# Performance work log

Measured on AMD Instinct MI355X. Metric: run time of the kernel, lower is better.

The kernel has to match this reference:

```python
import jax, jax.numpy as jnp
import numpy as np

N_NODES = 100000
N_EDGES = 1600000
N_GRAPHS = 128
F_IN = 4
H = 128
OUT = 2


def setup_inputs() -> dict:
    key = jax.random.key(0)
    ks = jax.random.split(key, 32)
    inp = {}
    inp["node_attr"] = jax.random.normal(ks[0], (N_NODES, F_IN), dtype=jnp.float32)
    inp["edge_index"] = jax.random.randint(ks[1], (2, N_EDGES), 0, N_NODES, dtype=jnp.int64)
    inp["batch"] = jnp.sort(jax.random.randint(ks[2], (N_NODES,), 0, N_GRAPHS, dtype=jnp.int64))
    # GraphConv params: lin_rel (weight+bias) applied to aggregated msgs, lin_root (no bias)
    dims = [(F_IN, H), (H, H), (H, H), (H, H)]
    for i, (din, dout) in enumerate(dims):
        s = 1.0 / np.sqrt(din)
        inp[f"Wr{i}"] = jax.random.uniform(ks[3 + 3 * i], (din, dout), jnp.float32, -s, s)
        inp[f"br{i}"] = jax.random.uniform(ks[4 + 3 * i], (dout,), jnp.float32, -s, s)
        inp[f"Wo{i}"] = jax.random.uniform(ks[5 + 3 * i], (din, dout), jnp.float32, -s, s)
    s = 1.0 / np.sqrt(H)
    for j, name in enumerate(["5", "6", "7", "8"]):
        inp[f"W{name}"] = jax.random.uniform(ks[16 + 2 * j], (H, H), jnp.float32, -s, s)
        inp[f"b{name}"] = jax.random.uniform(ks[17 + 2 * j], (H,), jnp.float32, -s, s)
    inp["Wl"] = jax.random.uniform(ks[30], (H, OUT), jnp.float32, -s, s)
    inp["bl"] = jax.random.uniform(ks[31], (OUT,), jnp.float32, -s, s)
    return inp


def _graph_conv(x, src, dst, Wr, br, Wo):
    # PyG GraphConv (aggr='add'): out = lin_rel(sum_{j->i} x_j) + lin_root(x_i)
    agg = jax.ops.segment_sum(x[src], dst, num_segments=N_NODES)
    return agg @ Wr + br + x @ Wo


def reference(node_attr, edge_index, batch,
              Wr0, br0, Wo0, Wr1, br1, Wo1, Wr2, br2, Wo2, Wr3, br3, Wo3,
              W5, b5, W6, b6, W7, b7, W8, b8, Wl, bl):
    src, dst = edge_index[0], edge_index[1]
    x = node_attr
    for Wr, br, Wo in [(Wr0, br0, Wo0), (Wr1, br1, Wo1), (Wr2, br2, Wo2), (Wr3, br3, Wo3)]:
        x = jax.nn.relu(_graph_conv(x, src, dst, Wr, br, Wo))
    # global mean pool over graphs
    sums = jax.ops.segment_sum(x, batch, num_segments=N_GRAPHS)
    cnt = jax.ops.segment_sum(jnp.ones((N_NODES,), x.dtype), batch, num_segments=N_GRAPHS)
    g = sums / jnp.maximum(cnt, 1.0)[:, None]
    # dropout p=0.5 is identity in eval mode
    g = jax.nn.relu(g @ W5 + b5)
    g = jax.nn.relu(g @ W6 + b6)
    g = jax.nn.relu(g @ W7 + b7)
    g = jax.nn.relu(g @ W8 + b8)
    return jax.nn.sigmoid(g @ Wl + bl)
```

## Files before the change

kernel.cpp:

```cpp
#include <hip/hip_runtime.h>
#include <hip/hip_bf16.h>
#include <math.h>

#define NN 100000
#define NE 1600000
#define NG 128
#define H 128
#define DMAX 64
#define NB 391
#define BCAP 5120
#define EPB 3125

typedef __attribute__((ext_vector_type(8))) short short8;
typedef __attribute__((ext_vector_type(4))) float floatx4;
typedef __attribute__((ext_vector_type(2))) float floatx2;
typedef __attribute__((ext_vector_type(4))) int intx4;
typedef __attribute__((ext_vector_type(4))) unsigned uintx4;
typedef __attribute__((ext_vector_type(2))) unsigned uintx2;


__global__ void k_init_wcvt(int* __restrict__ gbase, float* __restrict__ gsum,
                            unsigned* __restrict__ rowF8a, unsigned* __restrict__ rowF8b,
                            const float* __restrict__ Wr1, const float* __restrict__ Wo1,
                            const float* __restrict__ Wr2, const float* __restrict__ Wo2,
                            const float* __restrict__ Wr3, const float* __restrict__ Wo3,
                            __hip_bfloat16* __restrict__ wf) {
  if (blockIdx.x < 384) {
    int t = blockIdx.x * 256 + threadIdx.x;
    int L = t >> 15, tt = t & 32767;
    const float* Wr = (L == 0) ? Wr1 : (L == 1) ? Wr2 : Wr3;
    const float* Wo = (L == 0) ? Wo1 : (L == 1) ? Wo2 : Wo3;
    int j = tt & 7, lanex = (tt >> 3) & 63, ct = (tt >> 9) & 7, kt = tt >> 12;
    int lr = lanex & 15, quad = lanex >> 4;
    int n = ct * 16 + lr;
    int r = kt * 32 + quad * 8 + j;
    float v = (r < 128) ? Wr[r * 128 + n] : Wo[(r - 128) * 128 + n];
    wf[t] = __float2bfloat16(v);
  } else {
    int t = (blockIdx.x - 384) * 256 + threadIdx.x;
    if (t < NB) gbase[t] = 0;
    else if (t < NB + NG * H) gsum[t - NB] = 0.f;
    else if (t < NB + NG * H + 32) rowF8a[t - NB - NG * H] = 0u;
    else if (t < NB + NG * H + 64) rowF8b[t - NB - NG * H - 32] = 0u;
  }
}

__global__ __launch_bounds__(256) void k_bucket(const int* __restrict__ ei,
                                                int* __restrict__ gbase,
                                                int2* __restrict__ pairs) {
  __shared__ int scnt[512];
  __shared__ int soff[NB];
  __shared__ int sbase[NB];
  __shared__ int2 stg[EPB];
  __shared__ short sbkt[EPB];
  const int tid = threadIdx.x;
  const int e0 = blockIdx.x * EPB;
  const int* dst = ei + NE;

  scnt[tid] = 0;
  scnt[tid + 256] = 0;
  __syncthreads();
  for (int e = e0 + tid; e < e0 + EPB; e += 256) {
    int d = __builtin_nontemporal_load(dst + e);
    atomicAdd(&scnt[d >> 8], 1);
  }
  __syncthreads();
  int c0 = scnt[tid], c1 = scnt[tid + 256];
  for (int off = 1; off < 512; off <<= 1) {
    int v0 = (tid >= off) ? scnt[tid - off] : 0;
    int v1 = (tid + 256 >= off) ? scnt[tid + 256 - off] : 0;
    __syncthreads();
    scnt[tid] += v0;
    scnt[tid + 256] += v1;
    __syncthreads();
  }
  if (tid < NB) {
    soff[tid] = scnt[tid] - c0;
    sbase[tid] = c0 ? atomicAdd(&gbase[tid], c0) : 0;
  }
  if (tid + 256 < NB) {
    soff[tid + 256] = scnt[tid + 256] - c1;
    sbase[tid + 256] = c1 ? atomicAdd(&gbase[tid + 256], c1) : 0;
  }
  __syncthreads();
  scnt[tid] = 0;
  scnt[tid + 256] = 0;
  __syncthreads();
  for (int e = e0 + tid; e < e0 + EPB; e += 256) {
    int d = __builtin_nontemporal_load(dst + e);
    int s = __builtin_nontemporal_load(ei + e);
    int b = d >> 8;
    int p = soff[b] + atomicAdd(&scnt[b], 1);
    stg[p] = make_int2(s, d);
    sbkt[p] = (short)b;
  }
  __syncthreads();
  for (int i = tid; i < EPB; i += 256) {
    int b = sbkt[i];
    int gpos = sbase[b] + (i - soff[b]);
    if (gpos < BCAP) pairs[(size_t)b * BCAP + gpos] = stg[i];
  }
}

__global__ __launch_bounds__(256) void k_fill2(const int2* __restrict__ pairs,
                                               const int* __restrict__ gbase,
                                               int* __restrict__ fcnt,
                                               int* __restrict__ colp) {
  __shared__ int scnt[256];
  const int b = blockIdx.x;
  const int d0 = b << 8;
  const int tid = threadIdx.x;
  scnt[tid] = 0;
  __syncthreads();
  int n = gbase[b];
  if (n > BCAP) n = BCAP;
  const int2* pp = pairs + (size_t)b * BCAP;
  for (int e = tid; e < n; e += 256) {
    int2 sd = pp[e];
    int dl = sd.y - d0;
    int pos = atomicAdd(&scnt[dl], 1);
    if (pos < DMAX) colp[((size_t)(d0 + dl) << 6) + pos] = sd.x;
  }
  __syncthreads();
  int d = d0 + tid;
  if (d < NN) {
    int c = scnt[tid];
    fcnt[d] = (c > DMAX) ? DMAX : c;
  }
}

__device__ inline unsigned pk_bf16(float a, float b) {
  unsigned ua = __float_as_uint(a), ub = __float_as_uint(b);
  ua = (ua + 0x7fffu + ((ua >> 16) & 1u)) >> 16;
  ub = (ub + 0x7fffu + ((ub >> 16) & 1u)) & 0xffff0000u;
  return ua | ub;
}

__device__ inline void accf8(float* a, uint2 u) {
  floatx2 p;
  p = __builtin_amdgcn_cvt_pk_f32_fp8((int)u.x, false); a[0] += p.x; a[1] += p.y;
  p = __builtin_amdgcn_cvt_pk_f32_fp8((int)u.x, true);  a[2] += p.x; a[3] += p.y;
  p = __builtin_amdgcn_cvt_pk_f32_fp8((int)u.y, false); a[4] += p.x; a[5] += p.y;
  p = __builtin_amdgcn_cvt_pk_f32_fp8((int)u.y, true);  a[6] += p.x; a[7] += p.y;
}

__device__ inline short8 f8x8_bf16(uintx2 u) {
  floatx2 p0 = __builtin_amdgcn_cvt_pk_f32_fp8((int)u.x, false);
  floatx2 p1 = __builtin_amdgcn_cvt_pk_f32_fp8((int)u.x, true);
  floatx2 p2 = __builtin_amdgcn_cvt_pk_f32_fp8((int)u.y, false);
  floatx2 p3 = __builtin_amdgcn_cvt_pk_f32_fp8((int)u.y, true);
  union { uintx4 u; short8 s; } cv;
  cv.u.x = (__float_as_uint(p0.y) & 0xffff0000u) | (__float_as_uint(p0.x) >> 16);
  cv.u.y = (__float_as_uint(p1.y) & 0xffff0000u) | (__float_as_uint(p1.x) >> 16);
  cv.u.z = (__float_as_uint(p2.y) & 0xffff0000u) | (__float_as_uint(p2.x) >> 16);
  cv.u.w = (__float_as_uint(p3.y) & 0xffff0000u) | (__float_as_uint(p3.x) >> 16);
  return cv.s;
}

__global__ void k_aggf8(const uint2* __restrict__ xf8, const int* __restrict__ fcnt,
                        const int* __restrict__ colp, uintx4* __restrict__ agg) {
  int w = (blockIdx.x * blockDim.x + threadIdx.x) >> 6;
  int lane = threadIdx.x & 63;
  int qr = lane >> 4, ql = lane & 15;
  int node = 4 * w + qr;
  if (node >= NN) return;
  int cnt = fcnt[node];
  cnt = (cnt + 3) & ~3;
  const int* cp = colp + (node << 6);
  float a0[8] = {0}, a1[8] = {0}, a2[8] = {0}, a3[8] = {0};
  for (int i = 0; i < cnt; i += 4) {
    intx4 ss = __builtin_nontemporal_load((const intx4*)(cp + i));
    uint2 u0 = xf8[(size_t)ss.x * 16 + ql];
    uint2 u1 = xf8[(size_t)ss.y * 16 + ql];
    uint2 u2 = xf8[(size_t)ss.z * 16 + ql];
    uint2 u3 = xf8[(size_t)ss.w * 16 + ql];
    accf8(a0, u0);
    accf8(a1, u1);
    accf8(a2, u2);
    accf8(a3, u3);
  }
  float s[8];
#pragma unroll
  for (int t = 0; t < 8; ++t) s[t] = (a0[t] + a1[t]) + (a2[t] + a3[t]);
  uintx4 o;
  o.x = pk_bf16(s[0], s[1]);
  o.y = pk_bf16(s[2], s[3]);
  o.z = pk_bf16(s[4], s[5]);
  o.w = pk_bf16(s[6], s[7]);
  __builtin_nontemporal_store(o, agg + (size_t)node * 16 + ql);
}

__global__ void k_agg4b(const float* __restrict__ x, const int* __restrict__ fcnt,
                        int* __restrict__ colp, float* __restrict__ agg4) {
  int t = blockIdx.x * blockDim.x + threadIdx.x;
  int node = t >> 2, q = t & 3;
  if (node >= NN) return;
  int cnt = fcnt[node];
  int up = (cnt + 3) & ~3;
  int pi = cnt + q;
  if (pi < up) colp[(node << 6) + pi] = NN;
  const int* cp = colp + (node << 6);
  float4 acc = make_float4(0.f, 0.f, 0.f, 0.f);
  for (int e = q; e < cnt; e += 4) {
    float4 v = ((const float4*)x)[cp[e]];
    acc.x += v.x; acc.y += v.y; acc.z += v.z; acc.w += v.w;
  }
#pragma unroll
  for (int d = 1; d < 4; d <<= 1) {
    acc.x += __shfl_xor(acc.x, d);
    acc.y += __shfl_xor(acc.y, d);
    acc.z += __shfl_xor(acc.z, d);
    acc.w += __shfl_xor(acc.w, d);
  }
  if (q == 0) ((float4*)agg4)[node] = acc;
}

__global__ __launch_bounds__(256) void k_gemm4(
    const float* __restrict__ agg4, const float* __restrict__ x4,
    const float* __restrict__ Wr, const float* __restrict__ Wo,
    const float* __restrict__ br, unsigned char* __restrict__ out8) {
  __shared__ float sWr[512], sWo[512], sbr[128];
  int tid = threadIdx.x;
  sWr[tid] = Wr[tid]; sWr[tid + 256] = Wr[tid + 256];
  sWo[tid] = Wo[tid]; sWo[tid + 256] = Wo[tid + 256];
  if (tid < 128) sbr[tid] = br[tid];
  __syncthreads();
  int node = blockIdx.x * 16 + (tid >> 4);
  int j0 = (tid & 15) * 8;
  float4 a = ((const float4*)agg4)[node];
  float4 xv = ((const float4*)x4)[node];
  float4 b0 = *(const float4*)&sbr[j0];
  float4 b1 = *(const float4*)&sbr[j0 + 4];
  float v[8] = {b0.x, b0.y, b0.z, b0.w, b1.x, b1.y, b1.z, b1.w};
#pragma unroll
  for (int k = 0; k < 4; ++k) {
    float ak = (k == 0) ? a.x : (k == 1) ? a.y : (k == 2) ? a.z : a.w;
    float xk = (k == 0) ? xv.x : (k == 1) ? xv.y : (k == 2) ? xv.z : xv.w;
    float4 wr0 = *(const float4*)&sWr[k * 128 + j0];
    float4 wr1 = *(const float4*)&sWr[k * 128 + j0 + 4];
    float4 wo0 = *(const float4*)&sWo[k * 128 + j0];
    float4 wo1 = *(const float4*)&sWo[k * 128 + j0 + 4];
    v[0] = fmaf(ak, wr0.x, fmaf(xk, wo0.x, v[0]));
    v[1] = fmaf(ak, wr0.y, fmaf(xk, wo0.y, v[1]));
    v[2] = fmaf(ak, wr0.z, fmaf(xk, wo0.z, v[2]));
    v[3] = fmaf(ak, wr0.w, fmaf(xk, wo0.w, v[3]));
    v[4] = fmaf(ak, wr1.x, fmaf(xk, wo1.x, v[4]));
    v[5] = fmaf(ak, wr1.y, fmaf(xk, wo1.y, v[5]));
    v[6] = fmaf(ak, wr1.z, fmaf(xk, wo1.z, v[6]));
    v[7] = fmaf(ak, wr1.w, fmaf(xk, wo1.w, v[7]));
  }
#pragma unroll
  for (int jj = 0; jj < 8; ++jj) v[jj] = fmaxf(v[jj], 0.f);
  unsigned w8a, w8b;
  w8a = (unsigned)__builtin_amdgcn_cvt_pk_fp8_f32(v[0], v[1], 0, false);
  w8a = (unsigned)__builtin_amdgcn_cvt_pk_fp8_f32(v[2], v[3], (int)w8a, true);
  w8b = (unsigned)__builtin_amdgcn_cvt_pk_fp8_f32(v[4], v[5], 0, false);
  w8b = (unsigned)__builtin_amdgcn_cvt_pk_fp8_f32(v[6], v[7], (int)w8b, true);
  uint2 o8; o8.x = w8a; o8.y = w8b;
  *(uint2*)(out8 + (size_t)node * H + j0) = o8;
}

__global__ __launch_bounds__(256) void k_gemm_mfma(
    const __hip_bfloat16* __restrict__ A, const unsigned char* __restrict__ X8,
    const __hip_bfloat16* __restrict__ Wf, const float* __restrict__ br,
    unsigned char* __restrict__ out8) {
  __shared__ short8 sw[4096];
  const int tid = threadIdx.x;
  const int wv = tid >> 6, lane = tid & 63;
  const int quad = lane >> 4, lr = lane & 15;
  const int mbase = blockIdx.x * 128 + wv * 32;

#pragma unroll
  for (int i = 0; i < 16; ++i)
    sw[i * 256 + tid] = ((const short8*)Wf)[i * 256 + tid];

  floatx4 acc[2][8];
#pragma unroll
  for (int rt = 0; rt < 2; ++rt)
#pragma unroll
    for (int ct = 0; ct < 8; ++ct) acc[rt][ct] = (floatx4){0.f, 0.f, 0.f, 0.f};

  int r0 = mbase + lr;      if (r0 > NN - 1) r0 = NN - 1;
  int r1 = mbase + 16 + lr; if (r1 > NN - 1) r1 = NN - 1;

  __syncthreads();

#pragma unroll
  for (int kt = 0; kt < 8; ++kt) {
    const size_t koff = (size_t)(kt & 3) * 32 + quad * 8;
    short8 a0, a1;
    if (kt < 4) {
      a0 = __builtin_nontemporal_load((const short8*)(A + (size_t)r0 * H + koff));
      a1 = __builtin_nontemporal_load((const short8*)(A + (size_t)r1 * H + koff));
    } else {
      a0 = f8x8_bf16(__builtin_nontemporal_load((const uintx2*)(X8 + (size_t)r0 * H + koff)));
      a1 = f8x8_bf16(__builtin_nontemporal_load((const uintx2*)(X8 + (size_t)r1 * H + koff)));
    }
#pragma unroll
    for (int ct = 0; ct < 8; ++ct) {
      short8 b = sw[kt * 512 + ct * 64 + lane];
      acc[0][ct] = __builtin_amdgcn_mfma_f32_16x16x32_bf16(b, a0, acc[0][ct], 0, 0, 0);
      acc[1][ct] = __builtin_amdgcn_mfma_f32_16x16x32_bf16(b, a1, acc[1][ct], 0, 0, 0);
    }
  }

  floatx4 bias4[8];
#pragma unroll
  for (int ct = 0; ct < 8; ++ct)
    bias4[ct] = *(const floatx4*)(br + ct * 16 + quad * 4);

#pragma unroll
  for (int rt = 0; rt < 2; ++rt) {
    int row = mbase + rt * 16 + lr;
    if (row < NN) {
#pragma unroll
      for (int ct = 0; ct < 8; ++ct) {
        float v0 = fmaxf(acc[rt][ct][0] + bias4[ct].x, 0.f);
        float v1 = fmaxf(acc[rt][ct][1] + bias4[ct].y, 0.f);
        float v2 = fmaxf(acc[rt][ct][2] + bias4[ct].z, 0.f);
        float v3 = fmaxf(acc[rt][ct][3] + bias4[ct].w, 0.f);
        unsigned w8 = 0;
        w8 = (unsigned)__builtin_amdgcn_cvt_pk_fp8_f32(v0, v1, (int)w8, false);
        w8 = (unsigned)__builtin_amdgcn_cvt_pk_fp8_f32(v2, v3, (int)w8, true);
        *(unsigned*)(out8 + (size_t)row * H + ct * 16 + quad * 4) = w8;
      }
    }
  }
}

__global__ __launch_bounds__(256) void k_gemm_mfma_pool(
    const __hip_bfloat16* __restrict__ A, const unsigned char* __restrict__ X8,
    const __hip_bfloat16* __restrict__ Wf, const float* __restrict__ br,
    const int* __restrict__ batch, float* __restrict__ gsum) {
  __shared__ short8 sw[4096];
  __shared__ float pool[4][2][H];
  const int tid = threadIdx.x;
  const int wv = tid >> 6, lane = tid & 63;
  const int quad = lane >> 4, lr = lane & 15;
  const int bbase = blockIdx.x * 128;
  const int mbase = bbase + wv * 32;

#pragma unroll
  for (int i = 0; i < 16; ++i)
    sw[i * 256 + tid] = ((const short8*)Wf)[i * 256 + tid];

  floatx4 acc[2][8];
#pragma unroll
  for (int rt = 0; rt < 2; ++rt)
#pragma unroll
    for (int ct = 0; ct < 8; ++ct) acc[rt][ct] = (floatx4){0.f, 0.f, 0.f, 0.f};

  int r0 = mbase + lr;      if (r0 > NN - 1) r0 = NN - 1;
  int r1 = mbase + 16 + lr; if (r1 > NN - 1) r1 = NN - 1;

  __syncthreads();

#pragma unroll
  for (int kt = 0; kt < 8; ++kt) {
    const size_t koff = (size_t)(kt & 3) * 32 + quad * 8;
    short8 a0, a1;
    if (kt < 4) {
      a0 = __builtin_nontemporal_load((const short8*)(A + (size_t)r0 * H + koff));
      a1 = __builtin_nontemporal_load((const short8*)(A + (size_t)r1 * H + koff));
    } else {
      a0 = f8x8_bf16(__builtin_nontemporal_load((const uintx2*)(X8 + (size_t)r0 * H + koff)));
      a1 = f8x8_bf16(__builtin_nontemporal_load((const uintx2*)(X8 + (size_t)r1 * H + koff)));
    }
#pragma unroll
    for (int ct = 0; ct < 8; ++ct) {
      short8 b = sw[kt * 512 + ct * 64 + lane];
      acc[0][ct] = __builtin_amdgcn_mfma_f32_16x16x32_bf16(a0, b, acc[0][ct], 0, 0, 0);
      acc[1][ct] = __builtin_amdgcn_mfma_f32_16x16x32_bf16(a1, b, acc[1][ct], 0, 0, 0);
    }
  }

  const int g0 = batch[bbase];
  float bias[8];
#pragma unroll
  for (int ct = 0; ct < 8; ++ct) bias[ct] = br[ct * 16 + lr];

  float ps0[8] = {0.f, 0.f, 0.f, 0.f, 0.f, 0.f, 0.f, 0.f};
  float ps1[8] = {0.f, 0.f, 0.f, 0.f, 0.f, 0.f, 0.f, 0.f};
#pragma unroll
  for (int rt = 0; rt < 2; ++rt) {
#pragma unroll
    for (int rg = 0; rg < 4; ++rg) {
      int row = mbase + rt * 16 + quad * 4 + rg;
      if (row < NN) {
        if (batch[row] == g0) {
#pragma unroll
          for (int ct = 0; ct < 8; ++ct)
            ps0[ct] += fmaxf(acc[rt][ct][rg] + bias[ct], 0.f);
        } else {
#pragma unroll
          for (int ct = 0; ct < 8; ++ct)
            ps1[ct] += fmaxf(acc[rt][ct][rg] + bias[ct], 0.f);
        }
      }
    }
  }

#pragma unroll
  for (int ct = 0; ct < 8; ++ct) {
    float a = ps0[ct];
    a += __shfl_xor(a, 16);
    a += __shfl_xor(a, 32);
    float b = ps1[ct];
    b += __shfl_xor(b, 16);
    b += __shfl_xor(b, 32);
    if (quad == 0) {
      pool[wv][0][ct * 16 + lr] = a;
      pool[wv][1][ct * 16 + lr] = b;
    }
  }
  __syncthreads();

  if (tid < H) {
    float v = pool[0][0][tid] + pool[1][0][tid] + pool[2][0][tid] + pool[3][0][tid];
    atomicAdd(&gsum[g0 * H + tid], v);
    int rlast = bbase + 127; if (rlast > NN - 1) rlast = NN - 1;
    int g1 = batch[rlast];
    if (g1 != g0) {
      float w = pool[0][1][tid] + pool[1][1][tid] + pool[2][1][tid] + pool[3][1][tid];
      atomicAdd(&gsum[g1 * H + tid], w);
    }
  }
}

__global__ void k_head2(const float* __restrict__ gsum, const int* __restrict__ batch,
                        const float* __restrict__ W5, const float* __restrict__ b5,
                        const float* __restrict__ W6, const float* __restrict__ b6,
                        const float* __restrict__ W7, const float* __restrict__ b7,
                        const float* __restrict__ W8, const float* __restrict__ b8,
                        const float* __restrict__ Wl, const float* __restrict__ bl,
                        float* __restrict__ out) {
  __shared__ float s0[128], s1[128];
  __shared__ int sb[2];
  const int g = blockIdx.x, j = threadIdx.x;
  if (j < 2) {
    int tgt = g + j, lo = 0, hi = NN;
    while (lo < hi) {
      int mid = (lo + hi) >> 1;
      if (batch[mid] < tgt) lo = mid + 1; else hi = mid;
    }
    sb[j] = lo;
  }
  __syncthreads();
  float cnt = (float)(sb[1] - sb[0]);
  s0[j] = gsum[g * 128 + j] / fmaxf(cnt, 1.f);
  __syncthreads();
  const float* Ws[4] = {W5, W6, W7, W8};
  const float* bs[4] = {b5, b6, b7, b8};
  float* cur = s0;
  float* nxt = s1;
  for (int L = 0; L < 4; ++L) {
    const float* W = Ws[L];
    float a = bs[L][j];
    for (int k = 0; k < 128; ++k) a = fmaf(cur[k], W[k * 128 + j], a);
    nxt[j] = fmaxf(a, 0.f);
    __syncthreads();
    float* t = cur; cur = nxt; nxt = t;
  }
  if (j < 2) {
    float a = bl[j];
    for (int k = 0; k < 128; ++k) a = fmaf(cur[k], Wl[k * 2 + j], a);
    out[g * 2 + j] = 1.f / (1.f + __expf(-a));
  }
}

static inline char* ws_take(char*& p, size_t bytes) {
  char* r = p;
  p += (bytes + 255) & ~(size_t)255;
  return r;
}

extern "C" void kernel_launch(void* const* d_in, const int* in_sizes, int n_in,
                              void* d_out, int out_size, void* d_ws, size_t ws_size,
                              hipStream_t stream) {
  const float* x0 = (const float*)d_in[0];
  const int* ei = (const int*)d_in[1];
  const int* batch = (const int*)d_in[2];
  const float* Wr[4] = {(const float*)d_in[3], (const float*)d_in[6],
                        (const float*)d_in[9], (const float*)d_in[12]};
  const float* brr[4] = {(const float*)d_in[4], (const float*)d_in[7],
                         (const float*)d_in[10], (const float*)d_in[13]};
  const float* Wo[4] = {(const float*)d_in[5], (const float*)d_in[8],
                        (const float*)d_in[11], (const float*)d_in[14]};
  const float* W5 = (const float*)d_in[15];
  const float* b5 = (const float*)d_in[16];
  const float* W6 = (const float*)d_in[17];
  const float* b6 = (const float*)d_in[18];
  const float* W7 = (const float*)d_in[19];
  const float* b7 = (const float*)d_in[20];
  const float* W8 = (const float*)d_in[21];
  const float* b8 = (const float*)d_in[22];
  const float* Wl = (const float*)d_in[23];
  const float* bl = (const float*)d_in[24];
  float* out = (float*)d_out;

  char* p = (char*)d_ws;
  int* fcnt = (int*)ws_take(p, (size_t)NN * 4);
  int* colp = (int*)ws_take(p, (size_t)NN * DMAX * 4);
  __hip_bfloat16* agg = (__hip_bfloat16*)ws_take(p, (size_t)NN * H * 2);
  unsigned char* f8a = (unsigned char*)ws_take(p, (size_t)(NN + 1) * H);
  unsigned char* f8b = (unsigned char*)ws_take(p, (size_t)(NN + 1) * H);
  float* agg4 = (float*)ws_take(p, (size_t)NN * 4 * 4);
  float* gsum = (float*)ws_take(p, (size_t)NG * H * 4);
  __hip_bfloat16* wfall = (__hip_bfloat16*)ws_take(p, 3 * 32768 * 2);
  int* gbase = (int*)ws_take(p, NB * 4);
  __hip_bfloat16* wf1 = wfall;
  __hip_bfloat16* wf2 = wfall + 32768;
  __hip_bfloat16* wf3 = wfall + 65536;
  int2* pairs = (int2*)agg;
  (void)ws_size; (void)in_sizes; (void)n_in; (void)out_size;

  k_init_wcvt<<<384 + (NB + NG * H + 64 + 255) / 256, 256, 0, stream>>>(
      gbase, gsum, (unsigned*)(f8a + (size_t)NN * H), (unsigned*)(f8b + (size_t)NN * H),
      Wr[1], Wo[1], Wr[2], Wo[2], Wr[3], Wo[3], wfall);
  k_bucket<<<512, 256, 0, stream>>>(ei, gbase, pairs);
  k_fill2<<<NB, 256, 0, stream>>>(pairs, gbase, fcnt, colp);

  k_agg4b<<<(NN * 4 + 255) / 256, 256, 0, stream>>>(x0, fcnt, colp, agg4);
  k_gemm4<<<NN / 16, 256, 0, stream>>>(agg4, x0, Wr[0], Wo[0], brr[0], f8a);

  k_aggf8<<<6250, 256, 0, stream>>>((const uint2*)f8a, fcnt, colp, (uintx4*)agg);
  k_gemm_mfma<<<782, 256, 0, stream>>>(agg, f8a, wf1, brr[1], f8b);
  k_aggf8<<<6250, 256, 0, stream>>>((const uint2*)f8b, fcnt, colp, (uintx4*)agg);
  k_gemm_mfma<<<782, 256, 0, stream>>>(agg, f8b, wf2, brr[2], f8a);
  k_aggf8<<<6250, 256, 0, stream>>>((const uint2*)f8a, fcnt, colp, (uintx4*)agg);
  k_gemm_mfma_pool<<<782, 256, 0, stream>>>(agg, f8a, wf3, brr[3], batch, gsum);

  k_head2<<<NG, 128, 0, stream>>>(gsum, batch, W5, b5, W6, b6, W7, b7, W8, b8, Wl, bl, out);
}
```

Before: 376.1 us.

## Fuse layer-1 aggregation with its GEMM, prefetch MFMA A-operands, split bucketing finer

Merges the first-layer 4-feature neighbour aggregation and its small dense transform into one kernel, using 16 lanes per node and dropping the agg4 intermediate buffer and one launch. The MFMA GEMM kernels now issue all A-row and fp8 X-row loads up front, before the weight tile is staged into shared memory, so global latency overlaps the LDS fill. Edge bucketing uses 1024 blocks of about 1563 edges instead of 512, with bounds checks for the tail. The prefetch raises register pressure, and finer bucketing adds more global atomics on the bucket bases.

```diff
diff --git a/kernel.cpp b/kernel.cpp
--- a/kernel.cpp
+++ b/kernel.cpp
@@ -9,7 +9,8 @@
 #define DMAX 64
 #define NB 391
 #define BCAP 5120
-#define EPB 3125
+#define NBK 1024
+#define EPB 1563
 
 typedef __attribute__((ext_vector_type(8))) short short8;
 typedef __attribute__((ext_vector_type(4))) float floatx4;
@@ -55,12 +56,14 @@
   __shared__ short sbkt[EPB];
   const int tid = threadIdx.x;
   const int e0 = blockIdx.x * EPB;
+  int eend = e0 + EPB; if (eend > NE) eend = NE;
+  const int nloc = eend - e0;
   const int* dst = ei + NE;
 
   scnt[tid] = 0;
   scnt[tid + 256] = 0;
   __syncthreads();
-  for (int e = e0 + tid; e < e0 + EPB; e += 256) {
+  for (int e = e0 + tid; e < eend; e += 256) {
     int d = __builtin_nontemporal_load(dst + e);
     atomicAdd(&scnt[d >> 8], 1);
   }
@@ -86,7 +89,7 @@
   scnt[tid] = 0;
   scnt[tid + 256] = 0;
   __syncthreads();
-  for (int e = e0 + tid; e < e0 + EPB; e += 256) {
+  for (int e = e0 + tid; e < eend; e += 256) {
     int d = __builtin_nontemporal_load(dst + e);
     int s = __builtin_nontemporal_load(ei + e);
     int b = d >> 8;
@@ -95,7 +98,7 @@
     sbkt[p] = (short)b;
   }
   __syncthreads();
-  for (int i = tid; i < EPB; i += 256) {
+  for (int i = tid; i < nloc; i += 256) {
     int b = sbkt[i];
     int gpos = sbase[b] + (i - soff[b]);
     if (gpos < BCAP) pairs[(size_t)b * BCAP + gpos] = stg[i];
@@ -190,51 +193,48 @@
   __builtin_nontemporal_store(o, agg + (size_t)node * 16 + ql);
 }
 
-__global__ void k_agg4b(const float* __restrict__ x, const int* __restrict__ fcnt,
-                        int* __restrict__ colp, float* __restrict__ agg4) {
-  int t = blockIdx.x * blockDim.x + threadIdx.x;
-  int node = t >> 2, q = t & 3;
-  if (node >= NN) return;
-  int cnt = fcnt[node];
-  int up = (cnt + 3) & ~3;
-  int pi = cnt + q;
-  if (pi < up) colp[(node << 6) + pi] = NN;
+__global__ __launch_bounds__(256) void k_l1(
+    const float* __restrict__ x, const int* __restrict__ fcnt,
+    int* __restrict__ colp,
+    const float* __restrict__ Wr, const float* __restrict__ Wo,
+    const float* __restrict__ br, unsigned char* __restrict__ out8) {
+  __shared__ float sWr[512], sWo[512], sbr[128];
+  const int tid = threadIdx.x;
+  sWr[tid] = Wr[tid]; sWr[tid + 256] = Wr[tid + 256];
+  sWo[tid] = Wo[tid]; sWo[tid + 256] = Wo[tid + 256];
+  if (tid < 128) sbr[tid] = br[tid];
+
+  const int node = blockIdx.x * 16 + (tid >> 4);
+  const int q = tid & 15;
+  const int cnt = fcnt[node];
+  if (q < 4) {
+    int up = (cnt + 3) & ~3;
+    int pi = cnt + q;
+    if (pi < up) colp[(node << 6) + pi] = NN;
+  }
   const int* cp = colp + (node << 6);
   float4 acc = make_float4(0.f, 0.f, 0.f, 0.f);
-  for (int e = q; e < cnt; e += 4) {
+  for (int e = q; e < cnt; e += 16) {
     float4 v = ((const float4*)x)[cp[e]];
     acc.x += v.x; acc.y += v.y; acc.z += v.z; acc.w += v.w;
   }
 #pragma unroll
-  for (int d = 1; d < 4; d <<= 1) {
+  for (int d = 1; d < 16; d <<= 1) {
     acc.x += __shfl_xor(acc.x, d);
     acc.y += __shfl_xor(acc.y, d);
     acc.z += __shfl_xor(acc.z, d);
     acc.w += __shfl_xor(acc.w, d);
   }
-  if (q == 0) ((float4*)agg4)[node] = acc;
-}
-
-__global__ __launch_bounds__(256) void k_gemm4(
-    const float* __restrict__ agg4, const float* __restrict__ x4,
-    const float* __restrict__ Wr, const float* __restrict__ Wo,
-    const float* __restrict__ br, unsigned char* __restrict__ out8) {
-  __shared__ float sWr[512], sWo[512], sbr[128];
-  int tid = threadIdx.x;
-  sWr[tid] = Wr[tid]; sWr[tid + 256] = Wr[tid + 256];
-  sWo[tid] = Wo[tid]; sWo[tid + 256] = Wo[tid + 256];
-  if (tid < 128) sbr[tid] = br[tid];
-  __syncthreads();
-  int node = blockIdx.x * 16 + (tid >> 4);
-  int j0 = (tid & 15) * 8;
-  float4 a = ((const float4*)agg4)[node];
-  float4 xv = ((const float4*)x4)[node];
+  float4 xv = ((const float4*)x)[node];
+  __syncthreads();
+
+  const int j0 = q * 8;
   float4 b0 = *(const float4*)&sbr[j0];
   float4 b1 = *(const float4*)&sbr[j0 + 4];
   float v[8] = {b0.x, b0.y, b0.z, b0.w, b1.x, b1.y, b1.z, b1.w};
 #pragma unroll
   for (int k = 0; k < 4; ++k) {
-    float ak = (k == 0) ? a.x : (k == 1) ? a.y : (k == 2) ? a.z : a.w;
+    float ak = (k == 0) ? acc.x : (k == 1) ? acc.y : (k == 2) ? acc.z : acc.w;
     float xk = (k == 0) ? xv.x : (k == 1) ? xv.y : (k == 2) ? xv.z : xv.w;
     float4 wr0 = *(const float4*)&sWr[k * 128 + j0];
     float4 wr1 = *(const float4*)&sWr[k * 128 + j0 + 4];
@@ -270,6 +270,24 @@
   const int quad = lane >> 4, lr = lane & 15;
   const int mbase = blockIdx.x * 128 + wv * 32;
 
+  int r0 = mbase + lr;      if (r0 > NN - 1) r0 = NN - 1;
+  int r1 = mbase + 16 + lr; if (r1 > NN - 1) r1 = NN - 1;
+
+  short8 a0r[4], a1r[4];
+  uintx2 x0r[4], x1r[4];
+#pragma unroll
+  for (int k = 0; k < 4; ++k) {
+    const size_t koff = (size_t)k * 32 + quad * 8;
+    a0r[k] = __builtin_nontemporal_load((const short8*)(A + (size_t)r0 * H + koff));
+    a1r[k] = __builtin_nontemporal_load((const short8*)(A + (size_t)r1 * H + koff));
+  }
+#pragma unroll
+  for (int k = 0; k < 4; ++k) {
+    const size_t koff = (size_t)k * 32 + quad * 8;
+    x0r[k] = __builtin_nontemporal_load((const uintx2*)(X8 + (size_t)r0 * H + koff));
+    x1r[k] = __builtin_nontemporal_load((const uintx2*)(X8 + (size_t)r1 * H + koff));
+  }
+
 #pragma unroll
   for (int i = 0; i < 16; ++i)
     sw[i * 256 + tid] = ((const short8*)Wf)[i * 256 + tid];
@@ -280,22 +298,12 @@
 #pragma unroll
     for (int ct = 0; ct < 8; ++ct) acc[rt][ct] = (floatx4){0.f, 0.f, 0.f, 0.f};
 
-  int r0 = mbase + lr;      if (r0 > NN - 1) r0 = NN - 1;
-  int r1 = mbase + 16 + lr; if (r1 > NN - 1) r1 = NN - 1;
-
   __syncthreads();
 
 #pragma unroll
   for (int kt = 0; kt < 8; ++kt) {
-    const size_t koff = (size_t)(kt & 3) * 32 + quad * 8;
-    short8 a0, a1;
-    if (kt < 4) {
-      a0 = __builtin_nontemporal_load((const short8*)(A + (size_t)r0 * H + koff));
-      a1 = __builtin_nontemporal_load((const short8*)(A + (size_t)r1 * H + koff));
-    } else {
-      a0 = f8x8_bf16(__builtin_nontemporal_load((const uintx2*)(X8 + (size_t)r0 * H + koff)));
-      a1 = f8x8_bf16(__builtin_nontemporal_load((const uintx2*)(X8 + (size_t)r1 * H + koff)));
-    }
+    short8 a0 = (kt < 4) ? a0r[kt] : f8x8_bf16(x0r[kt - 4]);
+    short8 a1 = (kt < 4) ? a1r[kt] : f8x8_bf16(x1r[kt - 4]);
 #pragma unroll
     for (int ct = 0; ct < 8; ++ct) {
       short8 b = sw[kt * 512 + ct * 64 + lane];
@@ -340,6 +348,24 @@
   const int bbase = blockIdx.x * 128;
   const int mbase = bbase + wv * 32;
 
+  int r0 = mbase + lr;      if (r0 > NN - 1) r0 = NN - 1;
+  int r1 = mbase + 16 + lr; if (r1 > NN - 1) r1 = NN - 1;
+
+  short8 a0r[4], a1r[4];
+  uintx2 x0r[4], x1r[4];
+#pragma unroll
+  for (int k = 0; k < 4; ++k) {
+    const size_t koff = (size_t)k * 32 + quad * 8;
+    a0r[k] = __builtin_nontemporal_load((const short8*)(A + (size_t)r0 * H + koff));
+    a1r[k] = __builtin_nontemporal_load((const short8*)(A + (size_t)r1 * H + koff));
+  }
+#pragma unroll
+  for (int k = 0; k < 4; ++k) {
+    const size_t koff = (size_t)k * 32 + quad * 8;
+    x0r[k] = __builtin_nontemporal_load((const uintx2*)(X8 + (size_t)r0 * H + koff));
+    x1r[k] = __builtin_nontemporal_load((const uintx2*)(X8 + (size_t)r1 * H + koff));
+  }
+
 #pragma unroll
   for (int i = 0; i < 16; ++i)
     sw[i * 256 + tid] = ((const short8*)Wf)[i * 256 + tid];
@@ -350,22 +376,12 @@
 #pragma unroll
     for (int ct = 0; ct < 8; ++ct) acc[rt][ct] = (floatx4){0.f, 0.f, 0.f, 0.f};
 
-  int r0 = mbase + lr;      if (r0 > NN - 1) r0 = NN - 1;
-  int r1 = mbase + 16 + lr; if (r1 > NN - 1) r1 = NN - 1;
-
   __syncthreads();
 
 #pragma unroll
   for (int kt = 0; kt < 8; ++kt) {
-    const size_t koff = (size_t)(kt & 3) * 32 + quad * 8;
-    short8 a0, a1;
-    if (kt < 4) {
-      a0 = __builtin_nontemporal_load((const short8*)(A + (size_t)r0 * H + koff));
-      a1 = __builtin_nontemporal_load((const short8*)(A + (size_t)r1 * H + koff));
-    } else {
-      a0 = f8x8_bf16(__builtin_nontemporal_load((const uintx2*)(X8 + (size_t)r0 * H + koff)));
-      a1 = f8x8_bf16(__builtin_nontemporal_load((const uintx2*)(X8 + (size_t)r1 * H + koff)));
-    }
+    short8 a0 = (kt < 4) ? a0r[kt] : f8x8_bf16(x0r[kt - 4]);
+    short8 a1 = (kt < 4) ? a1r[kt] : f8x8_bf16(x1r[kt - 4]);
 #pragma unroll
     for (int ct = 0; ct < 8; ++ct) {
       short8 b = sw[kt * 512 + ct * 64 + lane];
@@ -504,7 +520,6 @@
   __hip_bfloat16* agg = (__hip_bfloat16*)ws_take(p, (size_t)NN * H * 2);
   unsigned char* f8a = (unsigned char*)ws_take(p, (size_t)(NN + 1) * H);
   unsigned char* f8b = (unsigned char*)ws_take(p, (size_t)(NN + 1) * H);
-  float* agg4 = (float*)ws_take(p, (size_t)NN * 4 * 4);
   float* gsum = (float*)ws_take(p, (size_t)NG * H * 4);
   __hip_bfloat16* wfall = (__hip_bfloat16*)ws_take(p, 3 * 32768 * 2);
   int* gbase = (int*)ws_take(p, NB * 4);
@@ -517,11 +532,10 @@
   k_init_wcvt<<<384 + (NB + NG * H + 64 + 255) / 256, 256, 0, stream>>>(
       gbase, gsum, (unsigned*)(f8a + (size_t)NN * H), (unsigned*)(f8b + (size_t)NN * H),
       Wr[1], Wo[1], Wr[2], Wo[2], Wr[3], Wo[3], wfall);
-  k_bucket<<<512, 256, 0, stream>>>(ei, gbase, pairs);
+  k_bucket<<<NBK, 256, 0, stream>>>(ei, gbase, pairs);
   k_fill2<<<NB, 256, 0, stream>>>(pairs, gbase, fcnt, colp);
 
-  k_agg4b<<<(NN * 4 + 255) / 256, 256, 0, stream>>>(x0, fcnt, colp, agg4);
-  k_gemm4<<<NN / 16, 256, 0, stream>>>(agg4, x0, Wr[0], Wo[0], brr[0], f8a);
+  k_l1<<<NN / 16, 256, 0, stream>>>(x0, fcnt, colp, Wr[0], Wo[0], brr[0], f8a);
 
   k_aggf8<<<6250, 256, 0, stream>>>((const uint2*)f8a, fcnt, colp, (uintx4*)agg);
   k_gemm_mfma<<<782, 256, 0, stream>>>(agg, f8a, wf1, brr[1], f8b);
```

Result: slower. 384.8 us (+2.3%).
